# Performance work log

Measured on AMD Instinct MI355X. Metric: run time of the kernel, lower is better.

Reference implementation:

```python
import jax, jax.numpy as jnp
import numpy as np

B, N, D, H = 8, 512, 1024, 16
HD = D // H
NI = 4          # num_instances == num_instances_per_batch
MAXI = 16       # max_instances
SCALE = HD ** -0.5


def _rms(t, w, eps=1e-6):
    return t * jax.lax.rsqrt(jnp.mean(t * t, axis=-1, keepdims=True) + eps) * w


def _lin(t, W, b):
    return t @ W + b


def _heads(t):
    b, n = t.shape[0], t.shape[1]
    return t.reshape(b, n, H, HD).transpose(0, 2, 1, 3)  # [b, H, n, hd]


def setup_inputs() -> dict:
    key = jax.random.key(0)
    ks = iter(jax.random.split(key, 16))

    def w(shape):
        return jax.random.normal(next(ks), shape, dtype=jnp.float32) * 0.02

    return {
        "x": jax.random.normal(next(ks), (B, N, D), dtype=jnp.float32),
        "instance_mask": jax.random.uniform(next(ks), (B, N, NI), dtype=jnp.float32),
        "Wq": w((D, D)), "bq": jnp.zeros((D,), jnp.float32),
        "Wk": w((D, D)), "bk": jnp.zeros((D,), jnp.float32),
        "Wv": w((D, D)), "bv": jnp.zeros((D,), jnp.float32),
        "Wo": w((D, D)), "bo": jnp.zeros((D,), jnp.float32),
        "Wiq": w((D, D)), "biq": jnp.zeros((D,), jnp.float32),
        "Wik": w((D, D)), "bik": jnp.zeros((D,), jnp.float32),
        "instance_embed": w((1, MAXI, D)),
        "qnorm_w": jnp.ones((HD,), jnp.float32),
        "knorm_w": jnp.ones((HD,), jnp.float32),
        "num_instances": NI,
        "num_instances_per_batch": NI,
    }


def reference(x, instance_mask, Wq, bq, Wk, bk, Wv, bv, Wo, bo,
              Wiq, biq, Wik, bik, instance_embed, qnorm_w, knorm_w,
              num_instances, num_instances_per_batch):
    # QKV projections + per-head QK-RMSNorm
    q = _rms(_heads(_lin(x, Wq, bq)), qnorm_w)   # [B,H,N,hd]
    k = _rms(_heads(_lin(x, Wk, bk)), knorm_w)
    v = _heads(_lin(x, Wv, bv))
    ni = num_instances                           # == num_instances_per_batch here,
    G = B // num_instances_per_batch             # so no leftover self-attn sub-branch;
    # (the module's initial global attention output is overwritten by this branch)
    qg = q.reshape(G, ni, H, N, HD)
    kg = k.reshape(G, ni, H, N, HD).transpose(0, 2, 1, 3, 4).reshape(G, H, ni * N, HD)
    vg = v.reshape(G, ni, H, N, HD).transpose(0, 2, 1, 3, 4).reshape(G, H, ni * N, HD)
    scores = jnp.einsum('gihnd,ghmd->gihnm', qg, kg) * SCALE  # [G,ni,H,N,ni*N]
    p = jax.nn.softmax(scores, axis=-1)
    og = jnp.einsum('gihnm,ghmd->gihnd', p, vg)
    out = og.reshape(B, H, N, HD).transpose(0, 2, 1, 3).reshape(B, N, D)
    # instance-embedding gate
    inst_feat = jnp.einsum('bnk,kd->bnd', instance_mask, instance_embed[0, :ni])
    iq = _heads(_lin(out, Wiq, biq))
    ik = _heads(_lin(inst_feat, Wik, bik))
    # mean over heads folded into the einsum (same math as mean of per-head scores)
    inst_attn = jax.nn.sigmoid(jnp.einsum('bhnd,bhmd->bnm', iq, ik) * (SCALE / H))
    gate = 1.0 + jnp.mean(inst_attn, axis=-1, keepdims=True)  # [B,N,1]
    return _lin(out * gate, Wo, bo)
```

## Files before the change

kernel.cpp:

```cpp
#include <hip/hip_runtime.h>
#include <cmath>

#define B_   8
#define N_   512
#define D_   1024
#define H_   16
#define HD_  64
#define NI_  4
#define BN_  (B_*N_)
#define KVLEN (NI_*N_)

typedef __attribute__((ext_vector_type(8)))  short  bf16x8;
typedef __attribute__((ext_vector_type(8)))  __bf16 bf16x8_t;
typedef __attribute__((ext_vector_type(16))) float  f32x16;
typedef __attribute__((ext_vector_type(4)))  short  s16x4;
typedef __attribute__((ext_vector_type(2)))  unsigned u32x2;

__device__ __forceinline__ short bf16_rn(float x) {
  unsigned u = __float_as_uint(x);
  unsigned r = (u + 0x7FFFu + ((u >> 16) & 1u)) >> 16;
  return (short)r;
}

__device__ __forceinline__ void split2(float x, short& hi, short& lo) {
  hi = bf16_rn(x);
  float h = __uint_as_float(((unsigned)(unsigned short)hi) << 16);
  float r = x - h;
  lo = bf16_rn(r);
}

__device__ __forceinline__ f32x16 mfma_bf16(bf16x8 a, bf16x8 b, f32x16 c) {
  return __builtin_amdgcn_mfma_f32_32x32x16_bf16(
      __builtin_bit_cast(bf16x8_t, a), __builtin_bit_cast(bf16x8_t, b), c, 0, 0, 0);
}

#define GLOAD16(gp, lp) __builtin_amdgcn_global_load_lds( \
  (const __attribute__((address_space(1))) unsigned*)(gp), \
  (__attribute__((address_space(3))) unsigned*)(lp), 16, 0, 0)

__device__ __forceinline__ long tiled_off(int row, int k) {
  return ((((long)(row >> 7) * 128 + (k >> 3)) * 128 + (row & 127)) * 8 + (k & 7));
}

__device__ __forceinline__ void xcd_swizzle(int& bx, int& by, int& bz) {
  const int gx = gridDim.x, gy = gridDim.y;
  const int nwg = gx * gy * gridDim.z;
  const int lin = blockIdx.x + gx * (blockIdx.y + gy * blockIdx.z);
  const int swz = (lin & 7) * (nwg >> 3) + (lin >> 3);
  bx = swz % gx;
  const int rest = swz / gx;
  by = rest % gy;
  bz = rest / gy;
}

__global__ __launch_bounds__(256) void wsplitAll(
    const float* __restrict__ Wq, const float* __restrict__ Wk,
    const float* __restrict__ Wv, const float* __restrict__ Wo,
    const float* __restrict__ x,
    short* __restrict__ QKVh, short* __restrict__ WoH,
    short* __restrict__ Xh)
{
  const int z = blockIdx.z;
  const int t  = threadIdx.x;
  if (z >= 4) {
    const int rowB = (z - 4) * 1024 + blockIdx.y * 64;
    const int colB = blockIdx.x * 64;
    const int r0 = t >> 4;
    const int c4 = t & 15;
    #pragma unroll
    for (int i = 0; i < 4; i++) {
      const int row = rowB + r0 + i * 16;
      float4 v = *(const float4*)&x[(long)row * D_ + colB + c4 * 4];
      short h[4];
      h[0] = bf16_rn(v.x);  h[1] = bf16_rn(v.y);
      h[2] = bf16_rn(v.z);  h[3] = bf16_rn(v.w);
      *(s16x4*)&Xh[tiled_off(row, colB + c4 * 4)] = *(s16x4*)h;
    }
    return;
  }
  __shared__ float tile[64][65];
  const float* W = (z == 0) ? Wq : (z == 1) ? Wk : (z == 2) ? Wv : Wo;
  const int kb = blockIdx.y * 64;
  const int cb = blockIdx.x * 64;
  const int r0 = t >> 4;
  const int c4 = t & 15;
  #pragma unroll
  for (int i = 0; i < 4; i++) {
    const int r = r0 + i * 16;
    *(float4*)&tile[r][c4 * 4] = *(const float4*)&W[(long)(kb + r) * D_ + cb + c4 * 4];
  }
  __syncthreads();
  #pragma unroll
  for (int i = 0; i < 4; i++) {
    const int c = r0 + i * 16;
    short hi[4];
    #pragma unroll
    for (int e = 0; e < 4; e++)
      hi[e] = bf16_rn(tile[c4 * 4 + e][c]);
    if (z < 3)
      *(s16x4*)&QKVh[tiled_off(z * D_ + cb + c, kb + c4 * 4)] = *(s16x4*)hi;
    else
      *(s16x4*)&WoH[tiled_off(cb + c, kb + c4 * 4)] = *(s16x4*)hi;
  }
}

__global__ __launch_bounds__(256) void fprep_p(
    const float* __restrict__ Wik, const float* __restrict__ emb,
    float* __restrict__ F4p)
{
  const int d  = blockIdx.x * 256 + threadIdx.x;
  const int eb = blockIdx.y;
  float s0 = 0, s1 = 0, s2 = 0, s3 = 0;
  for (int e = eb * 16; e < eb * 16 + 16; e++) {
    const float w = Wik[(long)e * D_ + d];
    s0 = fmaf(emb[e], w, s0);
    s1 = fmaf(emb[D_ + e], w, s1);
    s2 = fmaf(emb[2 * D_ + e], w, s2);
    s3 = fmaf(emb[3 * D_ + e], w, s3);
  }
  float* p = F4p + (long)eb * 4 * D_;
  p[d] = s0;  p[D_ + d] = s1;  p[2 * D_ + d] = s2;  p[3 * D_ + d] = s3;
}

__global__ __launch_bounds__(256) void freduce(
    const float* __restrict__ F4p, float* __restrict__ F4)
{
  const int i = blockIdx.x * 256 + threadIdx.x;
  float s = 0.f;
  #pragma unroll
  for (int eb = 0; eb < 64; eb++) s += F4p[(long)eb * 4096 + i];
  F4[i] = s;
}

__global__ __launch_bounds__(256) void hprep2(
    const float* __restrict__ Wiq, const float* __restrict__ F4,
    const float* __restrict__ bik, const float* __restrict__ biq,
    float* __restrict__ H5)
{
  __shared__ float red[4][5];
  const int t = threadIdx.x;
  const int blk = blockIdx.x;
  float s[5] = {0.f, 0.f, 0.f, 0.f, 0.f};
  const float* vr = (blk < 1024) ? Wiq + (long)blk * D_ : biq;
  for (int e = t; e < D_; e += 256) {
    const float w = vr[e];
    s[0] = fmaf(w, F4[e], s[0]);
    s[1] = fmaf(w, F4[D_ + e], s[1]);
    s[2] = fmaf(w, F4[2 * D_ + e], s[2]);
    s[3] = fmaf(w, F4[3 * D_ + e], s[3]);
    s[4] = fmaf(w, bik[e], s[4]);
  }
  #pragma unroll
  for (int j = 0; j < 5; j++)
    #pragma unroll
    for (int m = 1; m < 64; m <<= 1) s[j] += __shfl_xor(s[j], m);
  const int w64 = t >> 6, lane = t & 63;
  if (lane == 0)
    #pragma unroll
    for (int j = 0; j < 5; j++) red[w64][j] = s[j];
  __syncthreads();
  if (t < 5)
    H5[(long)blk * 5 + t] = red[0][t] + red[1][t] + red[2][t] + red[3][t];
}

template<int MODE, int SPLIT>
__global__ __launch_bounds__(256) void mfgemm2(
    const short* __restrict__ Ahi, const short* __restrict__ Alo,
    const short* __restrict__ Bhi,
    const float* __restrict__ b0, const float* __restrict__ b1,
    const float* __restrict__ b2,
    float* __restrict__ C, short* __restrict__ Vout,
    int bBlk, long sC, const float* __restrict__ gate_in)
{
  constexpr int NOPS = (SPLIT == 2) ? 3 : 2;
  __shared__ short lds[2][NOPS][4096];
  const int t = threadIdx.x, w = t >> 6, lane = t & 63;
  int bx, by, bz;
  xcd_swizzle(bx, by, bz);
  const int rowBase = by * 128;
  const int colBase = bx * 128;
  const long aoff = (long)by * 131072;
  const long boff = (long)(bz * bBlk + bx) * 131072;

  const short* mySrc;
  int op, half;
  if (SPLIT == 2) {
    op = (w < 3) ? w : 0; half = 0;
    mySrc = (w == 0) ? Ahi + aoff : (w == 1) ? Alo + aoff : Bhi + boff;
  } else {
    op = w >> 1; half = w & 1;
    mySrc = op ? Bhi + boff : Ahi + aoff;
  }

  auto stage = [&](int buf, int tt) {
    if (SPLIT == 2) {
      if (w == 3) return;
      const short* g = mySrc + ((long)tt * 512 + lane) * 8;
      #pragma unroll
      for (int i = 0; i < 8; i++)
        GLOAD16(g + i * 512, &lds[buf][op][i * 512]);
    } else {
      const short* g = mySrc + ((long)tt * 512 + half * 256 + lane) * 8;
      #pragma unroll
      for (int i = 0; i < 4; i++)
        GLOAD16(g + i * 512, &lds[buf][op][(half * 256 + i * 64) * 8]);
    }
  };

  const int wr = w >> 1, wc = w & 1;
  const int lrow = lane & 31, lk = lane >> 5;

  f32x16 acc[2][2] = {};

  auto compute = [&](int buf) {
    #pragma unroll
    for (int kh = 0; kh < 2; kh++) {
      const int kq = 2 * kh + lk;
      bf16x8 ah[2], bh[2];
      #pragma unroll
      for (int m = 0; m < 2; m++)
        ah[m] = *(const bf16x8*)&lds[buf][0][(kq * 128 + wr * 64 + m * 32 + lrow) * 8];
      #pragma unroll
      for (int n = 0; n < 2; n++)
        bh[n] = *(const bf16x8*)&lds[buf][(SPLIT == 2) ? 2 : 1][(kq * 128 + wc * 64 + n * 32 + lrow) * 8];
      if (SPLIT == 2) {
        bf16x8 al[2];
        #pragma unroll
        for (int m = 0; m < 2; m++)
          al[m] = *(const bf16x8*)&lds[buf][1][(kq * 128 + wr * 64 + m * 32 + lrow) * 8];
        #pragma unroll
        for (int m = 0; m < 2; m++)
          #pragma unroll
          for (int n = 0; n < 2; n++) {
            acc[m][n] = mfma_bf16(al[m], bh[n], acc[m][n]);
            acc[m][n] = mfma_bf16(ah[m], bh[n], acc[m][n]);
          }
      } else {
        #pragma unroll
        for (int m = 0; m < 2; m++)
          #pragma unroll
          for (int n = 0; n < 2; n++)
            acc[m][n] = mfma_bf16(ah[m], bh[n], acc[m][n]);
      }
    }
  };

  const int NT = 32;
  stage(0, 0);
  for (int tt = 0; tt < NT - 1; ++tt) {
    stage((tt + 1) & 1, tt + 1);
    if (SPLIT == 2) asm volatile("s_waitcnt vmcnt(8)" ::: "memory");
    else            asm volatile("s_waitcnt vmcnt(4)" ::: "memory");
    __builtin_amdgcn_s_barrier();
    __builtin_amdgcn_sched_barrier(0);
    compute(tt & 1);
    __builtin_amdgcn_s_barrier();
  }
  asm volatile("s_waitcnt vmcnt(0)" ::: "memory");
  __builtin_amdgcn_s_barrier();
  __builtin_amdgcn_sched_barrier(0);
  compute((NT - 1) & 1);

  const float* bias = (bz == 1) ? b1 : (bz == 2) ? b2 : b0;
  float bcol[2];
  #pragma unroll
  for (int n = 0; n < 2; n++)
    bcol[n] = bias[colBase + wc * 64 + n * 32 + lrow];

  if (MODE == 6 && bz == 2) {
    #pragma unroll
    for (int m = 0; m < 2; m++)
      #pragma unroll
      for (int r = 0; r < 16; r++) {
        const int row = rowBase + wr * 64 + m * 32 + (r & 3) + 8 * (r >> 2) + 4 * lk;
        const int bb = row >> 9, g = bb >> 2;
        const int kv = (bb & 3) * 512 + (row & 511);
        const int tile = kv >> 5, vkv = kv & 31;
        #pragma unroll
        for (int n = 0; n < 2; n++) {
          const int col = colBase + wc * 64 + n * 32 + lrow;
          const int h = col >> 6, dl = col & 63;
          const long idx = ((long)(g * H_ + h) * 64 + tile) * 2048
                         + dl * 32 + (((vkv >> 3) ^ ((dl >> 1) & 3)) * 8) + (vkv & 7);
          Vout[idx] = bf16_rn(acc[m][n][r] + bcol[n]);
        }
      }
    return;
  }

  float* Cb = C + (long)bz * sC;
  #pragma unroll
  for (int m = 0; m < 2; m++) {
    #pragma unroll
    for (int r = 0; r < 16; r++) {
      const int row = rowBase + wr * 64 + m * 32 + (r & 3) + 8 * (r >> 2) + 4 * lk;
      float g = 1.f;
      if (MODE == 2) g = gate_in[row];
      #pragma unroll
      for (int n = 0; n < 2; n++) {
        const int col = colBase + wc * 64 + n * 32 + lrow;
        Cb[(long)row * D_ + col] = acc[m][n][r] * g + bcol[n];
      }
    }
  }
}

__global__ __launch_bounds__(256) void kvprepK(
    const float* __restrict__ kf, const float* __restrict__ knw,
    short* __restrict__ Knb)
{
  const int tile = blockIdx.x, h = blockIdx.y, g = blockIdx.z;
  const int t = threadIdx.x;
  const int skv = t >> 3, sg = t & 7;
  const int m  = tile * 32 + skv;
  const int bb = g * NI_ + (m >> 9), nn = m & (N_ - 1);
  const float* kp = kf + ((long)(bb * N_ + nn)) * D_ + h * HD_ + sg * 8;
  float k8[8];
  *(float4*)&k8[0] = *(const float4*)&kp[0];
  *(float4*)&k8[4] = *(const float4*)&kp[4];
  float ks2 = 0.f;
  #pragma unroll
  for (int j = 0; j < 8; j++) ks2 += k8[j] * k8[j];
  ks2 += __shfl_xor(ks2, 1);
  ks2 += __shfl_xor(ks2, 2);
  ks2 += __shfl_xor(ks2, 4);
  const float kr = rsqrtf(ks2 * (1.f / 64.f) + 1e-6f);
  bf16x8 kb;
  #pragma unroll
  for (int j = 0; j < 8; j++) kb[j] = bf16_rn(k8[j] * kr * knw[sg * 8 + j]);
  *(bf16x8*)&Knb[((long)(g * H_ + h) * KVLEN + m) * 64 + ((sg ^ (m & 7)) * 8)] = kb;
}

__global__ __launch_bounds__(256) void attn3(
    const float* __restrict__ q, const short* __restrict__ Knb,
    const short* __restrict__ Vtb, const float* __restrict__ qnw,
    float* __restrict__ opart, float* __restrict__ lpart)
{
  int qb, h, bz;
  xcd_swizzle(qb, h, bz);
  const int b  = bz >> 1, s = bz & 1;
  const int g  = b >> 2;
  const int t  = threadIdx.x;
  const int w  = t >> 6;
  const int lane = t & 63;
  const int l31 = lane & 31, hi = lane >> 5;

  __shared__ short Kt[2][2048];
  __shared__ short Vt[2][2048];

  const int qrow = qb * 128 + w * 32 + l31;
  const float* qp = q + ((long)b * N_ + qrow) * D_ + h * HD_ + hi * 8;
  float qv[4][8];
  float ss = 0.f;
  #pragma unroll
  for (int c = 0; c < 4; c++) {
    *(float4*)&qv[c][0] = *(const float4*)&qp[c * 16];
    *(float4*)&qv[c][4] = *(const float4*)&qp[c * 16 + 4];
    #pragma unroll
    for (int j = 0; j < 8; j++) ss += qv[c][j] * qv[c][j];
  }
  ss += __shfl_xor(ss, 32);
  const float qr = rsqrtf(ss * (1.f / 64.f) + 1e-6f) * 0.1803368801111244f;
  bf16x8 qf[4];
  #pragma unroll
  for (int c = 0; c < 4; c++)
    #pragma unroll
    for (int j = 0; j < 8; j++)
      qf[c][j] = bf16_rn(qv[c][j] * qr * qnw[c * 16 + hi * 8 + j]);

  const short* Kg = Knb + (long)(g * H_ + h) * KVLEN * 64 + (long)s * 32 * 2048;
  const short* Vg = Vtb + (long)(g * H_ + h) * 64 * 2048 + (long)s * 32 * 2048;

  auto stage = [&](int buf, int i) {
    GLOAD16(Kg + (long)i * 2048 + t * 8, &Kt[buf][w * 512]);
    GLOAD16(Vg + (long)i * 2048 + t * 8, &Vt[buf][w * 512]);
  };

  f32x16 oacc[2] = {};
  float l = 0.f;

  stage(0, 0);
  for (int i = 0; i < 32; ++i) {
    const int buf = i & 1;
    if (i + 1 < 32) {
      stage(buf ^ 1, i + 1);
      asm volatile("s_waitcnt vmcnt(2)" ::: "memory");
    } else {
      asm volatile("s_waitcnt vmcnt(0)" ::: "memory");
    }
    __builtin_amdgcn_s_barrier();
    __builtin_amdgcn_sched_barrier(0);

    f32x16 sc = {};
    #pragma unroll
    for (int c = 0; c < 4; c++) {
      bf16x8 kfr = *(const bf16x8*)&Kt[buf][l31 * 64 + (((2 * c + hi) * 8) ^ ((l31 & 7) << 3))];
      sc = mfma_bf16(kfr, qf[c], sc);
    }
    float p[16];
    #pragma unroll
    for (int r = 0; r < 16; r++) {
      p[r] = exp2f(sc[r]);
      l += p[r];
    }
    unsigned wd[8];
    #pragma unroll
    for (int i2 = 0; i2 < 8; i2++)
      asm("v_cvt_pk_bf16_f32 %0, %1, %2" : "=v"(wd[i2]) : "v"(p[2 * i2]), "v"(p[2 * i2 + 1]));
    u32x2 r0 = __builtin_amdgcn_permlane32_swap(wd[0], wd[2], false, false);
    u32x2 r1 = __builtin_amdgcn_permlane32_swap(wd[1], wd[3], false, false);
    u32x2 r2 = __builtin_amdgcn_permlane32_swap(wd[4], wd[6], false, false);
    u32x2 r3 = __builtin_amdgcn_permlane32_swap(wd[5], wd[7], false, false);
    int4 f0 = { (int)r0.x, (int)r1.x, (int)r0.y, (int)r1.y };
    int4 f1 = { (int)r2.x, (int)r3.x, (int)r2.y, (int)r3.y };
    #pragma unroll
    for (int n = 0; n < 2; n++) {
      const int d = n * 32 + l31;
      const int fd = (d >> 1) & 3;
      bf16x8 v0 = *(const bf16x8*)&Vt[buf][d * 32 + ((hi ^ fd) * 8)];
      bf16x8 v1 = *(const bf16x8*)&Vt[buf][d * 32 + (((2 | hi) ^ fd) * 8)];
      oacc[n] = mfma_bf16(__builtin_bit_cast(bf16x8, f0), v0, oacc[n]);
      oacc[n] = mfma_bf16(__builtin_bit_cast(bf16x8, f1), v1, oacc[n]);
    }
    __builtin_amdgcn_s_barrier();
  }

  l += __shfl_xor(l, 32);
  #pragma unroll
  for (int r = 0; r < 16; r++) {
    const int qg = qb * 128 + w * 32 + (r & 3) + 8 * (r >> 2) + 4 * hi;
    float* op = opart + ((long)s * BN_ + b * N_ + qg) * D_ + h * HD_ + l31;
    op[0]  = oacc[0][r];
    op[32] = oacc[1][r];
  }
  if (hi == 0)
    lpart[((long)s * BN_ + b * N_ + qb * 128 + w * 32 + l31) * H_ + h] = l;
}

__global__ __launch_bounds__(256) void attn_reduce2(
    const float* __restrict__ opart, const float* __restrict__ lpart,
    const float* __restrict__ H5, const float* __restrict__ mask,
    short* __restrict__ ohi, short* __restrict__ olo,
    float* __restrict__ gate)
{
  __shared__ float red[4][5];
  __shared__ float Gs[5];
  __shared__ float sred[4];
  const int t = threadIdx.x;
  const int row = blockIdx.x;
  const int bb = row >> 9;
  const int col = t * 4;
  const int h   = col >> 6;
  const float l = lpart[(long)row * H_ + h] + lpart[((long)BN_ + row) * H_ + h];
  const float inv = 1.f / l;
  float4 a = *(const float4*)&opart[(long)row * D_ + col];
  float4 b = *(const float4*)&opart[((long)BN_ + row) * D_ + col];
  float o4[4] = { (a.x + b.x) * inv, (a.y + b.y) * inv,
                  (a.z + b.z) * inv, (a.w + b.w) * inv };
  short hh[4], ll[4];
  split2(o4[0], hh[0], ll[0]);
  split2(o4[1], hh[1], ll[1]);
  split2(o4[2], hh[2], ll[2]);
  split2(o4[3], hh[3], ll[3]);
  const long o = tiled_off(row, col);
  *(s16x4*)&ohi[o] = *(s16x4*)hh;
  *(s16x4*)&olo[o] = *(s16x4*)ll;
  float s[5] = {0.f, 0.f, 0.f, 0.f, 0.f};
  #pragma unroll
  for (int c = 0; c < 4; c++) {
    const float* hp = &H5[(long)(col + c) * 5];
    #pragma unroll
    for (int j = 0; j < 5; j++) s[j] = fmaf(o4[c], hp[j], s[j]);
  }
  #pragma unroll
  for (int j = 0; j < 5; j++)
    #pragma unroll
    for (int m = 1; m < 64; m <<= 1) s[j] += __shfl_xor(s[j], m);
  const int w64 = t >> 6, lane = t & 63;
  if (lane == 0)
    #pragma unroll
    for (int j = 0; j < 5; j++) red[w64][j] = s[j];
  __syncthreads();
  if (t < 5) Gs[t] = red[0][t] + red[1][t] + red[2][t] + red[3][t] + H5[5120 + t];
  __syncthreads();
  const float g0 = Gs[0], g1 = Gs[1], g2 = Gs[2], g3 = Gs[3], g4 = Gs[4];
  const float sc = 0.125f / 16.f;
  const float* mrow = mask + (long)bb * N_ * NI_;
  float sg = 0.f;
  #pragma unroll
  for (int q = 0; q < 2; q++) {
    const float4 mk = *(const float4*)&mrow[(t * 2 + q) * 4];
    const float z = fmaf(g0, mk.x, fmaf(g1, mk.y, fmaf(g2, mk.z, fmaf(g3, mk.w, g4))));
    sg += 1.f / (1.f + __expf(-z * sc));
  }
  #pragma unroll
  for (int m = 1; m < 64; m <<= 1) sg += __shfl_xor(sg, m);
  if (lane == 0) sred[w64] = sg;
  __syncthreads();
  if (t == 0)
    gate[row] = 1.f + (sred[0] + sred[1] + sred[2] + sred[3]) * (1.f / 512.f);
}

extern "C" void kernel_launch(void* const* d_in, const int* in_sizes, int n_in,
                              void* d_out, int out_size, void* d_ws, size_t ws_size,
                              hipStream_t stream)
{
  const float* x    = (const float*)d_in[0];
  const float* mask = (const float*)d_in[1];
  const float* Wq   = (const float*)d_in[2];
  const float* bq   = (const float*)d_in[3];
  const float* Wk   = (const float*)d_in[4];
  const float* bk   = (const float*)d_in[5];
  const float* Wv   = (const float*)d_in[6];
  const float* bv   = (const float*)d_in[7];
  const float* Wo   = (const float*)d_in[8];
  const float* bo   = (const float*)d_in[9];
  const float* Wiq  = (const float*)d_in[10];
  const float* biq  = (const float*)d_in[11];
  const float* Wik  = (const float*)d_in[12];
  const float* bik  = (const float*)d_in[13];
  const float* emb  = (const float*)d_in[14];
  const float* qnw  = (const float*)d_in[15];
  const float* knw  = (const float*)d_in[16];
  float* out = (float*)d_out;

  float* ws = (float*)d_ws;
  const size_t SZ = (size_t)BN_ * D_;
  float* qbuf = ws;
  float* kbuf = qbuf + SZ;
  float* vbuf = kbuf + SZ;
  float* opart = kbuf;
  short* ohi  = (short*)(vbuf + SZ);
  short* olo  = ohi + SZ;
  short* xhi  = (short*)(ws + 4 * SZ);
  short* xlo  = xhi + SZ;
  short* Knb  = xhi;
  short* Vtb  = xlo;
  short* Wbig_hi = (short*)(ws + 5 * SZ);
  short* Wbig_lo = Wbig_hi + (size_t)3 * D_ * D_;
  float* gate  = (float*)Wbig_hi;
  float* lpart = gate + BN_;
  short* WoH = Wbig_lo;
  float* F4  = (float*)(Wbig_lo + (size_t)D_ * D_);
  float* H5  = F4 + 4 * D_;
  float* F4p = H5 + 1025 * 5;

  const dim3 blk(256);

  fprep_p<<<dim3(4, 64), blk, 0, stream>>>(Wik, emb, F4p);
  freduce<<<dim3(16), blk, 0, stream>>>(F4p, F4);
  hprep2<<<dim3(1025), blk, 0, stream>>>(Wiq, F4, bik, biq, H5);

  wsplitAll<<<dim3(16, 16, 8), blk, 0, stream>>>(
      Wq, Wk, Wv, Wo, x, Wbig_hi, WoH, xhi);

  mfgemm2<6, 0><<<dim3(8, 32, 3), blk, 0, stream>>>(
      xhi, nullptr, Wbig_hi, bq, bk, bv,
      qbuf, Vtb, 8, (long)SZ, nullptr);

  kvprepK<<<dim3(KVLEN / 32, H_, 2), blk, 0, stream>>>(kbuf, knw, Knb);

  attn3<<<dim3(N_ / 128, H_, B_ * 2), blk, 0, stream>>>(
      qbuf, Knb, Vtb, qnw, opart, lpart);

  attn_reduce2<<<BN_, blk, 0, stream>>>(opart, lpart, H5, mask, ohi, olo, gate);

  mfgemm2<2, 2><<<dim3(8, 32, 1), blk, 0, stream>>>(
      ohi, olo, WoH, bo, nullptr, nullptr,
      out, nullptr, 0, 0, gate);
}
```

Measured before the change: 195.5 us.

## Drop hi/lo split for output projection and split attention KV three ways

The attention output is now rounded to a single bf16 copy instead of a hi+lo pair, so the output-projection GEMM does half the MFMAs and loads. Attention's KV split goes from 2 to 3 partitions, adding grid blocks for occupancy, and the reduce kernel sums three partials. The precision loss on the attention output may push the result closer to the tolerance. Buffer aliasing is also rearranged: ohi now reuses qbuf, and opart takes three partition slots starting at kbuf.

```diff
diff --git a/kernel.cpp b/kernel.cpp
--- a/kernel.cpp
+++ b/kernel.cpp
@@ -20,13 +20,6 @@
   unsigned u = __float_as_uint(x);
   unsigned r = (u + 0x7FFFu + ((u >> 16) & 1u)) >> 16;
   return (short)r;
-}
-
-__device__ __forceinline__ void split2(float x, short& hi, short& lo) {
-  hi = bf16_rn(x);
-  float h = __uint_as_float(((unsigned)(unsigned short)hi) << 16);
-  float r = x - h;
-  lo = bf16_rn(r);
 }
 
 __device__ __forceinline__ f32x16 mfma_bf16(bf16x8 a, bf16x8 b, f32x16 c) {
@@ -172,7 +165,7 @@
     float* __restrict__ C, short* __restrict__ Vout,
     int bBlk, long sC, const float* __restrict__ gate_in)
 {
-  constexpr int NOPS = (SPLIT == 2) ? 3 : 2;
+  constexpr int NOPS = 2;
   __shared__ short lds[2][NOPS][4096];
   const int t = threadIdx.x, w = t >> 6, lane = t & 63;
   int bx, by, bz;
@@ -182,29 +175,14 @@
   const long aoff = (long)by * 131072;
   const long boff = (long)(bz * bBlk + bx) * 131072;
 
-  const short* mySrc;
-  int op, half;
-  if (SPLIT == 2) {
-    op = (w < 3) ? w : 0; half = 0;
-    mySrc = (w == 0) ? Ahi + aoff : (w == 1) ? Alo + aoff : Bhi + boff;
-  } else {
-    op = w >> 1; half = w & 1;
-    mySrc = op ? Bhi + boff : Ahi + aoff;
-  }
+  const int op = w >> 1, half = w & 1;
+  const short* mySrc = op ? Bhi + boff : Ahi + aoff;
 
   auto stage = [&](int buf, int tt) {
-    if (SPLIT == 2) {
-      if (w == 3) return;
-      const short* g = mySrc + ((long)tt * 512 + lane) * 8;
-      #pragma unroll
-      for (int i = 0; i < 8; i++)
-        GLOAD16(g + i * 512, &lds[buf][op][i * 512]);
-    } else {
-      const short* g = mySrc + ((long)tt * 512 + half * 256 + lane) * 8;
-      #pragma unroll
-      for (int i = 0; i < 4; i++)
-        GLOAD16(g + i * 512, &lds[buf][op][(half * 256 + i * 64) * 8]);
-    }
+    const short* g = mySrc + ((long)tt * 512 + half * 256 + lane) * 8;
+    #pragma unroll
+    for (int i = 0; i < 4; i++)
+      GLOAD16(g + i * 512, &lds[buf][op][(half * 256 + i * 64) * 8]);
   };
 
   const int wr = w >> 1, wc = w & 1;
@@ -222,26 +200,12 @@
         ah[m] = *(const bf16x8*)&lds[buf][0][(kq * 128 + wr * 64 + m * 32 + lrow) * 8];
       #pragma unroll
       for (int n = 0; n < 2; n++)
-        bh[n] = *(const bf16x8*)&lds[buf][(SPLIT == 2) ? 2 : 1][(kq * 128 + wc * 64 + n * 32 + lrow) * 8];
-      if (SPLIT == 2) {
-        bf16x8 al[2];
+        bh[n] = *(const bf16x8*)&lds[buf][1][(kq * 128 + wc * 64 + n * 32 + lrow) * 8];
+      #pragma unroll
+      for (int m = 0; m < 2; m++)
         #pragma unroll
-        for (int m = 0; m < 2; m++)
-          al[m] = *(const bf16x8*)&lds[buf][1][(kq * 128 + wr * 64 + m * 32 + lrow) * 8];
-        #pragma unroll
-        for (int m = 0; m < 2; m++)
-          #pragma unroll
-          for (int n = 0; n < 2; n++) {
-            acc[m][n] = mfma_bf16(al[m], bh[n], acc[m][n]);
-            acc[m][n] = mfma_bf16(ah[m], bh[n], acc[m][n]);
-          }
-      } else {
-        #pragma unroll
-        for (int m = 0; m < 2; m++)
-          #pragma unroll
-          for (int n = 0; n < 2; n++)
-            acc[m][n] = mfma_bf16(ah[m], bh[n], acc[m][n]);
-      }
+        for (int n = 0; n < 2; n++)
+          acc[m][n] = mfma_bf16(ah[m], bh[n], acc[m][n]);
     }
   };
 
@@ -249,8 +213,7 @@
   stage(0, 0);
   for (int tt = 0; tt < NT - 1; ++tt) {
     stage((tt + 1) & 1, tt + 1);
-    if (SPLIT == 2) asm volatile("s_waitcnt vmcnt(8)" ::: "memory");
-    else            asm volatile("s_waitcnt vmcnt(4)" ::: "memory");
+    asm volatile("s_waitcnt vmcnt(4)" ::: "memory");
     __builtin_amdgcn_s_barrier();
     __builtin_amdgcn_sched_barrier(0);
     compute(tt & 1);
@@ -338,7 +301,7 @@
 {
   int qb, h, bz;
   xcd_swizzle(qb, h, bz);
-  const int b  = bz >> 1, s = bz & 1;
+  const int b  = bz / 3, s = bz - 3 * b;
   const int g  = b >> 2;
   const int t  = threadIdx.x;
   const int w  = t >> 6;
@@ -368,21 +331,24 @@
     for (int j = 0; j < 8; j++)
       qf[c][j] = bf16_rn(qv[c][j] * qr * qnw[c * 16 + hi * 8 + j]);
 
-  const short* Kg = Knb + (long)(g * H_ + h) * KVLEN * 64 + (long)s * 32 * 2048;
-  const short* Vg = Vtb + (long)(g * H_ + h) * 64 * 2048 + (long)s * 32 * 2048;
+  const short* Kg = Knb + (long)(g * H_ + h) * KVLEN * 64;
+  const short* Vg = Vtb + (long)(g * H_ + h) * 64 * 2048;
 
   auto stage = [&](int buf, int i) {
     GLOAD16(Kg + (long)i * 2048 + t * 8, &Kt[buf][w * 512]);
     GLOAD16(Vg + (long)i * 2048 + t * 8, &Vt[buf][w * 512]);
   };
 
+  const int it0 = (s * 64) / 3;
+  const int it1 = ((s + 1) * 64) / 3;
+
   f32x16 oacc[2] = {};
   float l = 0.f;
 
-  stage(0, 0);
-  for (int i = 0; i < 32; ++i) {
-    const int buf = i & 1;
-    if (i + 1 < 32) {
+  stage(0, it0);
+  for (int i = it0; i < it1; ++i) {
+    const int buf = (i - it0) & 1;
+    if (i + 1 < it1) {
       stage(buf ^ 1, i + 1);
       asm volatile("s_waitcnt vmcnt(2)" ::: "memory");
     } else {
@@ -440,8 +406,7 @@
 __global__ __launch_bounds__(256) void attn_reduce2(
     const float* __restrict__ opart, const float* __restrict__ lpart,
     const float* __restrict__ H5, const float* __restrict__ mask,
-    short* __restrict__ ohi, short* __restrict__ olo,
-    float* __restrict__ gate)
+    short* __restrict__ ohi, float* __restrict__ gate)
 {
   __shared__ float red[4][5];
   __shared__ float Gs[5];
@@ -451,26 +416,25 @@
   const int bb = row >> 9;
   const int col = t * 4;
   const int h   = col >> 6;
-  const float l = lpart[(long)row * H_ + h] + lpart[((long)BN_ + row) * H_ + h];
+  const float l = lpart[(long)row * H_ + h]
+                + lpart[((long)BN_ + row) * H_ + h]
+                + lpart[((long)2 * BN_ + row) * H_ + h];
   const float inv = 1.f / l;
   float4 a = *(const float4*)&opart[(long)row * D_ + col];
   float4 b = *(const float4*)&opart[((long)BN_ + row) * D_ + col];
-  float o4[4] = { (a.x + b.x) * inv, (a.y + b.y) * inv,
-                  (a.z + b.z) * inv, (a.w + b.w) * inv };
-  short hh[4], ll[4];
-  split2(o4[0], hh[0], ll[0]);
-  split2(o4[1], hh[1], ll[1]);
-  split2(o4[2], hh[2], ll[2]);
-  split2(o4[3], hh[3], ll[3]);
-  const long o = tiled_off(row, col);
-  *(s16x4*)&ohi[o] = *(s16x4*)hh;
-  *(s16x4*)&olo[o] = *(s16x4*)ll;
+  float4 c = *(const float4*)&opart[((long)2 * BN_ + row) * D_ + col];
+  float o4[4] = { (a.x + b.x + c.x) * inv, (a.y + b.y + c.y) * inv,
+                  (a.z + b.z + c.z) * inv, (a.w + b.w + c.w) * inv };
+  short hh[4];
+  hh[0] = bf16_rn(o4[0]);  hh[1] = bf16_rn(o4[1]);
+  hh[2] = bf16_rn(o4[2]);  hh[3] = bf16_rn(o4[3]);
+  *(s16x4*)&ohi[tiled_off(row, col)] = *(s16x4*)hh;
   float s[5] = {0.f, 0.f, 0.f, 0.f, 0.f};
   #pragma unroll
-  for (int c = 0; c < 4; c++) {
-    const float* hp = &H5[(long)(col + c) * 5];
-    #pragma unroll
-    for (int j = 0; j < 5; j++) s[j] = fmaf(o4[c], hp[j], s[j]);
+  for (int cc = 0; cc < 4; cc++) {
+    const float* hp = &H5[(long)(col + cc) * 5];
+    #pragma unroll
+    for (int j = 0; j < 5; j++) s[j] = fmaf(o4[cc], hp[j], s[j]);
   }
   #pragma unroll
   for (int j = 0; j < 5; j++)
@@ -528,10 +492,8 @@
   const size_t SZ = (size_t)BN_ * D_;
   float* qbuf = ws;
   float* kbuf = qbuf + SZ;
-  float* vbuf = kbuf + SZ;
   float* opart = kbuf;
-  short* ohi  = (short*)(vbuf + SZ);
-  short* olo  = ohi + SZ;
+  short* ohi  = (short*)qbuf;
   short* xhi  = (short*)(ws + 4 * SZ);
   short* xlo  = xhi + SZ;
   short* Knb  = xhi;
@@ -560,12 +522,12 @@
 
   kvprepK<<<dim3(KVLEN / 32, H_, 2), blk, 0, stream>>>(kbuf, knw, Knb);
 
-  attn3<<<dim3(N_ / 128, H_, B_ * 2), blk, 0, stream>>>(
+  attn3<<<dim3(N_ / 128, H_, B_ * 3), blk, 0, stream>>>(
       qbuf, Knb, Vtb, qnw, opart, lpart);
 
-  attn_reduce2<<<BN_, blk, 0, stream>>>(opart, lpart, H5, mask, ohi, olo, gate);
-
-  mfgemm2<2, 2><<<dim3(8, 32, 1), blk, 0, stream>>>(
-      ohi, olo, WoH, bo, nullptr, nullptr,
+  attn_reduce2<<<BN_, blk, 0, stream>>>(opart, lpart, H5, mask, ohi, gate);
+
+  mfgemm2<2, 0><<<dim3(8, 32, 1), blk, 0, stream>>>(
+      ohi, nullptr, WoH, bo, nullptr, nullptr,
       out, nullptr, 0, 0, gate);
 }
```

Result: faster. 188.7 us (-3.5%).
